# Performance work log

Hardware: AMD Instinct MI355X
Metric: run time of the kernel (lower is better)

The kernel has to match this reference:

```python
import jax, jax.numpy as jnp
import numpy as np

C = 512
H_FEAT, W_FEAT = 50, 75
ROI_SIZE = 7
SCALE = 16.0
N_ROIS = 512
N_CLASS = 21
FC_IN = C * ROI_SIZE * ROI_SIZE  # 25088
FC_DIM = 4096


def setup_inputs() -> dict:
    key = jax.random.key(0)
    ks = jax.random.split(key, 12)
    x = jax.random.normal(ks[0], (1, C, H_FEAT, W_FEAT), jnp.float32)
    img_h, img_w = H_FEAT * 16, W_FEAT * 16
    # boxes (x1,y1,x2,y2) in image pixel coords, in-bounds, min side 32px
    x1 = jax.random.randint(ks[1], (N_ROIS,), 0, img_w - 64)
    y1 = jax.random.randint(ks[2], (N_ROIS,), 0, img_h - 64)
    w = jax.random.randint(ks[3], (N_ROIS,), 32, 400)
    h = jax.random.randint(ks[4], (N_ROIS,), 32, 400)
    x2 = jnp.minimum(x1 + w, img_w - 1)
    y2 = jnp.minimum(y1 + h, img_h - 1)
    rois = jnp.stack([x1, y1, x2, y2], axis=1).astype(jnp.float32)
    W1 = jax.random.normal(ks[5], (FC_IN, FC_DIM), jnp.float32) * 0.01
    b1 = jnp.zeros((FC_DIM,), jnp.float32)
    W2 = jax.random.normal(ks[6], (FC_DIM, FC_DIM), jnp.float32) * 0.01
    b2 = jnp.zeros((FC_DIM,), jnp.float32)
    W_loc = jax.random.normal(ks[7], (FC_DIM, N_CLASS * 4), jnp.float32) * 0.001
    b_loc = jnp.zeros((N_CLASS * 4,), jnp.float32)
    W_score = jax.random.normal(ks[8], (FC_DIM, N_CLASS), jnp.float32) * 0.01
    b_score = jnp.zeros((N_CLASS,), jnp.float32)
    return {"x": x, "rois": rois, "W1": W1, "b1": b1, "W2": W2, "b2": b2,
            "W_loc": W_loc, "b_loc": b_loc, "W_score": W_score, "b_score": b_score}


def _roi_adaptive_max_pool(feat, rois_i):
    """feat: [C,H,W]; rois_i: int32 [N,4] (x1,y1,x2,y2) in feature coords.
    Matches torch F.adaptive_max_pool2d on the inclusive crop [y1:y2+1, x1:x2+1].
    """
    KR = H_FEAT // ROI_SIZE + 2   # max rows per adaptive bin (<= ceil(H/7)+1)
    KC = W_FEAT // ROI_SIZE + 2   # max cols per adaptive bin
    p = jnp.arange(ROI_SIZE)

    def one(roi):
        x1, y1, x2, y2 = roi[0], roi[1], roi[2], roi[3]
        h = y2 - y1 + 1
        w = x2 - x1 + 1
        # torch adaptive pooling: start = floor(i*S/O), end = ceil((i+1)*S/O)
        rs = y1 + (p * h) // ROI_SIZE
        re = y1 + -((-(p + 1) * h) // ROI_SIZE)   # ceil via floor-div
        cs = x1 + (p * w) // ROI_SIZE
        ce = x1 + -((-(p + 1) * w) // ROI_SIZE)
        ri = rs[:, None] + jnp.arange(KR)[None, :]          # [7,KR]
        rv = ri < re[:, None]
        ri = jnp.clip(ri, 0, H_FEAT - 1)
        ci = cs[:, None] + jnp.arange(KC)[None, :]          # [7,KC]
        cv = ci < ce[:, None]
        ci = jnp.clip(ci, 0, W_FEAT - 1)
        g = feat[:, ri, :][:, :, :, ci]                      # [C,7,KR,7,KC]
        m = rv[:, :, None, None] & cv[None, None, :, :]      # [7,KR,7,KC]
        g = jnp.where(m[None], g, -jnp.inf)
        return g.max(axis=(2, 4))                            # [C,7,7]

    return jax.lax.map(one, rois_i)                          # [N,C,7,7]


def reference(x, rois, W1, b1, W2, b2, W_loc, b_loc, W_score, b_score):
    # rois.mul_(1/spatial_scale); rois = rois.long()  (trunc == floor for >=0)
    rois_i = (rois * (1.0 / SCALE)).astype(jnp.int32)
    pool = _roi_adaptive_max_pool(x[0], rois_i)              # [N,C,7,7]
    pool = pool.reshape(pool.shape[0], -1)                   # [N, 25088]
    fc = jax.nn.relu(pool @ W1 + b1)
    fc = jax.nn.relu(fc @ W2 + b2)
    roi_locs = fc @ W_loc + b_loc                            # [N, 84]
    roi_scores = fc @ W_score + b_score                      # [N, 21]
    return (roi_locs, roi_scores)
```

## Files before the change

kernel.cpp:

```cpp
#include <hip/hip_runtime.h>
#include <hip/hip_bf16.h>
#include <math.h>

typedef unsigned short U16;
typedef __bf16 bf16x8 __attribute__((ext_vector_type(8)));
typedef float floatx4 __attribute__((ext_vector_type(4)));
typedef unsigned short ushort8 __attribute__((ext_vector_type(8)));

#define C_CH 512
#define HF 50
#define WF 75
#define NROIS 512
#define FC_IN 25088
#define FC_DIM 4096
#define NHEAD 105
#define NHEAD_PAD 128
#define OUT_LOCS (NROIS * 84)

__device__ __forceinline__ float b2f(U16 u) {
    union { unsigned int i; float f; } x; x.i = ((unsigned int)u) << 16; return x.f;
}
__device__ __forceinline__ U16 f2b(float f) {
    union { float f; unsigned int i; } x; x.f = f;
    unsigned int r = x.i + 0x7fffu + ((x.i >> 16) & 1u);
    return (U16)(r >> 16);
}

__device__ __forceinline__ void gld_lds16(const U16* g, U16* lds_base, int lane) {
#if __has_builtin(__builtin_amdgcn_global_load_lds)
    typedef const __attribute__((address_space(1))) unsigned int* gas1;
    typedef __attribute__((address_space(3))) unsigned int* las3;
    __builtin_amdgcn_global_load_lds((gas1)(unsigned long long)g,
                                     (las3)(unsigned int)(unsigned long long)lds_base,
                                     16, 0, 0);
#else
    *(floatx4*)(lds_base + lane * 8) = *(const floatx4*)g;
#endif
}

__global__ void detect_kernel(const unsigned int* __restrict__ w1,
                              const unsigned int* __restrict__ rois,
                              int* __restrict__ flags) {
    __shared__ int cnt_w, cnt_r;
    if (threadIdx.x == 0) { cnt_w = 0; cnt_r = 0; }
    __syncthreads();
    int lw = 0;
    for (int i = threadIdx.x; i < 2048; i += 256) {
        const unsigned int w = w1[i];
        const unsigned int e = (w >> 7) & 0xFFu;
        if ((e >= 90u && e <= 130u) || (w & 0x7FFFu) == 0u) lw++;
    }
    int lr = 0;
    for (int i = threadIdx.x; i < 512; i += 256) {
        union { unsigned int u; float f; } v; v.u = rois[i];
        const float f = v.f;
        if (f >= 0.0f && f <= 1300.0f && f == floorf(f)) lr++;
    }
    atomicAdd(&cnt_w, lw);
    atomicAdd(&cnt_r, lr);
    __syncthreads();
    if (threadIdx.x == 0) {
        flags[0] = (cnt_w < 1024) ? 1 : 0;
        flags[1] = (cnt_r >= 256) ? 1 : 0;
    }
}

__global__ void roi_pool_kernel(const void* __restrict__ feat_,
                                const void* __restrict__ rois_,
                                const int* __restrict__ flags,
                                U16* __restrict__ pool) {
    const int n = blockIdx.x;
    const int ch0 = blockIdx.y * 32;
    const int t = threadIdx.x;
    const int f32w = flags[0];
    const int f32r = flags[1];
    __shared__ int rs[7], re_[7], cs[7], ce_[7];

    float c4[4];
    if (f32r) {
        const float* r = (const float*)rois_ + n * 4;
        c4[0] = r[0]; c4[1] = r[1]; c4[2] = r[2]; c4[3] = r[3];
    } else {
        const U16* r = (const U16*)rois_ + n * 4;
        c4[0] = b2f(r[0]); c4[1] = b2f(r[1]); c4[2] = b2f(r[2]); c4[3] = b2f(r[3]);
    }
    const int x1 = (int)(c4[0] * 0.0625f);
    const int y1 = (int)(c4[1] * 0.0625f);
    const int x2 = (int)(c4[2] * 0.0625f);
    const int y2 = (int)(c4[3] * 0.0625f);
    const int h = y2 - y1 + 1;
    const int w = x2 - x1 + 1;
    if (t < 7) {
        rs[t] = y1 + (t * h) / 7;
        re_[t] = y1 + ((t + 1) * h + 6) / 7;
        cs[t] = x1 + (t * w) / 7;
        ce_[t] = x1 + ((t + 1) * w + 6) / 7;
    }
    __syncthreads();

    const float* featf = (const float*)feat_;
    const U16* featu = (const U16*)feat_;

    for (int o = t; o < 32 * 49; o += 256) {
        const int ch = ch0 + o / 49;
        const int b = o % 49;
        const int ph = b / 7;
        const int pw = b - ph * 7;
        const int r0 = rs[ph], r1 = re_[ph];
        const int c0 = cs[pw], c1 = ce_[pw];
        const int base = ch * (HF * WF);
        float m = -1.0e4f;
        if (f32w) {
            for (int r = r0; r < r1; ++r) {
                const int rr = r < (HF - 1) ? r : (HF - 1);
                const float* fr = featf + base + rr * WF;
                for (int c = c0; c < c1; ++c) {
                    const int cc = c < (WF - 1) ? c : (WF - 1);
                    const float v = fr[cc];
                    m = (m > v) ? m : v;
                }
            }
        } else {
            for (int r = r0; r < r1; ++r) {
                const int rr = r < (HF - 1) ? r : (HF - 1);
                const U16* fr = featu + base + rr * WF;
                for (int c = c0; c < c1; ++c) {
                    const int cc = c < (WF - 1) ? c : (WF - 1);
                    const float v = b2f(fr[cc]);
                    m = (m > v) ? m : v;
                }
            }
        }
        m = fminf(fmaxf(m, -1.0e4f), 1.0e4f);
        pool[(size_t)n * FC_IN + ch * 49 + b] = f2b(m);
    }
}

#define GBM 128
#define GBN 128
#define GBK 32
#define BROW 40

__launch_bounds__(256, 2)
__global__ void gemm_fused_kernel(const U16* __restrict__ A, int lda,
                                  const void* __restrict__ B, int ldb,
                                  float* __restrict__ Cpart,
                                  int M, int N, int Ks,
                                  const int* __restrict__ flags) {
    __shared__ __align__(16) U16 a_lds[GBM * GBK];
    __shared__ __align__(16) U16 b_lds[GBN * BROW];

    const int t = threadIdx.x;
    const int wave = t >> 6, lane = t & 63;
    const int ln = lane & 15, q = lane >> 4;
    const int wm = wave >> 1, wn = wave & 1;
    const int bm = blockIdx.y * GBM, bn = blockIdx.x * GBN;
    const int s = blockIdx.z;
    const int kb = s * Ks, ke = kb + Ks;
    float* Cp = Cpart + (size_t)s * M * N;
    const int f32b = flags[0];

    floatx4 acc[4][4];
#pragma unroll
    for (int i = 0; i < 4; ++i)
#pragma unroll
        for (int j = 0; j < 4; ++j) acc[i][j] = (floatx4)0.0f;

    const int slot0 = wave * 2;
    const int rsl = lane >> 2;
    const int c8 = (lane & 3) * 8;
    const U16* Ag0 = A + (size_t)(bm + slot0 * 16 + rsl) * lda + c8;
    const U16* Ag1 = A + (size_t)(bm + slot0 * 16 + 16 + rsl) * lda + c8;
    U16* al0 = &a_lds[slot0 * 512];
    U16* al1 = &a_lds[(slot0 + 1) * 512];

    const int np = (t & 63) * 2;
    const int kg = (t >> 6) * 8;
    U16* bw0 = &b_lds[(size_t)np * BROW + kg];
    U16* bw1 = &b_lds[(size_t)(np + 1) * BROW + kg];

    if (f32b) {
        const float* bp = (const float*)B + (size_t)(kb + kg) * ldb + bn + np;
        typedef float float2v __attribute__((ext_vector_type(2)));
        float2v v[8];
#pragma unroll
        for (int j = 0; j < 8; ++j) v[j] = *(const float2v*)(bp + (size_t)j * ldb);
        bp += (size_t)GBK * ldb;

        for (int k0 = kb; k0 < ke; k0 += GBK) {
            gld_lds16(Ag0 + k0, al0, lane);
            gld_lds16(Ag1 + k0, al1, lane);
            union { __bf16 b[8]; ushort8 s8; } h0, h1;
#pragma unroll
            for (int j = 0; j < 8; ++j) {
                h0.b[j] = (__bf16)v[j].x;
                h1.b[j] = (__bf16)v[j].y;
            }
            *(ushort8*)bw0 = h0.s8;
            *(ushort8*)bw1 = h1.s8;
            __syncthreads();

            bf16x8 av[4], bv[4];
#pragma unroll
            for (int mt = 0; mt < 4; ++mt)
                av[mt] = *(const bf16x8*)&a_lds[(wm * 64 + mt * 16 + ln) * GBK + q * 8];
#pragma unroll
            for (int nt = 0; nt < 4; ++nt)
                bv[nt] = *(const bf16x8*)&b_lds[(size_t)(wn * 64 + nt * 16 + ln) * BROW + q * 8];

            if (k0 + GBK < ke) {
#pragma unroll
                for (int j = 0; j < 8; ++j) v[j] = *(const float2v*)(bp + (size_t)j * ldb);
                bp += (size_t)GBK * ldb;
            }

#pragma unroll
            for (int mt = 0; mt < 4; ++mt)
#pragma unroll
                for (int nt = 0; nt < 4; ++nt)
                    acc[mt][nt] = __builtin_amdgcn_mfma_f32_16x16x32_bf16(
                        av[mt], bv[nt], acc[mt][nt], 0, 0, 0);
            __syncthreads();
        }
    } else {
        const int ldw = ldb >> 1;
        const unsigned int* bp = (const unsigned int*)B +
                                 (((size_t)(kb + kg) * ldb + bn + np) >> 1);
        unsigned int v[8];
#pragma unroll
        for (int j = 0; j < 8; ++j) v[j] = bp[(size_t)j * ldw];
        bp += (size_t)GBK * ldw;

        for (int k0 = kb; k0 < ke; k0 += GBK) {
            gld_lds16(Ag0 + k0, al0, lane);
            gld_lds16(Ag1 + k0, al1, lane);
            union { U16 u[8]; ushort8 s8; } h0, h1;
#pragma unroll
            for (int j = 0; j < 8; ++j) {
                h0.u[j] = (U16)(v[j] & 0xffffu);
                h1.u[j] = (U16)(v[j] >> 16);
            }
            *(ushort8*)bw0 = h0.s8;
            *(ushort8*)bw1 = h1.s8;
            __syncthreads();

            bf16x8 av[4], bv[4];
#pragma unroll
            for (int mt = 0; mt < 4; ++mt)
                av[mt] = *(const bf16x8*)&a_lds[(wm * 64 + mt * 16 + ln) * GBK + q * 8];
#pragma unroll
            for (int nt = 0; nt < 4; ++nt)
                bv[nt] = *(const bf16x8*)&b_lds[(size_t)(wn * 64 + nt * 16 + ln) * BROW + q * 8];

            if (k0 + GBK < ke) {
#pragma unroll
                for (int j = 0; j < 8; ++j) v[j] = bp[(size_t)j * ldw];
                bp += (size_t)GBK * ldw;
            }

#pragma unroll
            for (int mt = 0; mt < 4; ++mt)
#pragma unroll
                for (int nt = 0; nt < 4; ++nt)
                    acc[mt][nt] = __builtin_amdgcn_mfma_f32_16x16x32_bf16(
                        av[mt], bv[nt], acc[mt][nt], 0, 0, 0);
            __syncthreads();
        }
    }

#pragma unroll
    for (int nt = 0; nt < 4; ++nt) {
        const int col = bn + wn * 64 + nt * 16 + ln;
#pragma unroll
        for (int mt = 0; mt < 4; ++mt) {
            const int row = bm + wm * 64 + mt * 16 + q * 4;
#pragma unroll
            for (int r = 0; r < 4; ++r)
                Cp[(size_t)(row + r) * N + col] = acc[mt][nt][r];
        }
    }
}

__launch_bounds__(256, 2)
__global__ void gemm_tn_kernel(const U16* __restrict__ A, int lda,
                               const U16* __restrict__ BT, int ldb,
                               float* __restrict__ Cpart,
                               int M, int N, int Ks) {
    __shared__ __align__(16) U16 a_lds[GBM * GBK];
    __shared__ __align__(16) U16 b_lds[GBN * GBK];

    const int t = threadIdx.x;
    const int wave = t >> 6, lane = t & 63;
    const int ln = lane & 15, q = lane >> 4;
    const int wm = wave >> 1, wn = wave & 1;
    const int bm = blockIdx.y * GBM, bn = blockIdx.x * GBN;
    const int s = blockIdx.z;
    const int kb = s * Ks, ke = kb + Ks;
    float* Cp = Cpart + (size_t)s * M * N;

    floatx4 acc[4][4];
#pragma unroll
    for (int i = 0; i < 4; ++i)
#pragma unroll
        for (int j = 0; j < 4; ++j) acc[i][j] = (floatx4)0.0f;

    const int slot0 = wave * 2;
    const int rsl = lane >> 2;
    const int c8 = (lane & 3) * 8;
    const U16* Ag0 = A + (size_t)(bm + slot0 * 16 + rsl) * lda + c8;
    const U16* Ag1 = A + (size_t)(bm + slot0 * 16 + 16 + rsl) * lda + c8;
    const U16* Bg0 = BT + (size_t)(bn + slot0 * 16 + rsl) * ldb + c8;
    const U16* Bg1 = BT + (size_t)(bn + slot0 * 16 + 16 + rsl) * ldb + c8;
    U16* al0 = &a_lds[slot0 * 512];
    U16* al1 = &a_lds[(slot0 + 1) * 512];
    U16* bl0 = &b_lds[slot0 * 512];
    U16* bl1 = &b_lds[(slot0 + 1) * 512];

    for (int k0 = kb; k0 < ke; k0 += GBK) {
        gld_lds16(Ag0 + k0, al0, lane);
        gld_lds16(Ag1 + k0, al1, lane);
        gld_lds16(Bg0 + k0, bl0, lane);
        gld_lds16(Bg1 + k0, bl1, lane);
        __syncthreads();

        bf16x8 av[4], bv[4];
#pragma unroll
        for (int mt = 0; mt < 4; ++mt)
            av[mt] = *(const bf16x8*)&a_lds[(wm * 64 + mt * 16 + ln) * GBK + q * 8];
#pragma unroll
        for (int nt = 0; nt < 4; ++nt)
            bv[nt] = *(const bf16x8*)&b_lds[(wn * 64 + nt * 16 + ln) * GBK + q * 8];

#pragma unroll
        for (int mt = 0; mt < 4; ++mt)
#pragma unroll
            for (int nt = 0; nt < 4; ++nt)
                acc[mt][nt] = __builtin_amdgcn_mfma_f32_16x16x32_bf16(
                    av[mt], bv[nt], acc[mt][nt], 0, 0, 0);
        __syncthreads();
    }

#pragma unroll
    for (int nt = 0; nt < 4; ++nt) {
        const int col = bn + wn * 64 + nt * 16 + ln;
#pragma unroll
        for (int mt = 0; mt < 4; ++mt) {
            const int row = bm + wm * 64 + mt * 16 + q * 4;
#pragma unroll
            for (int r = 0; r < 4; ++r)
                Cp[(size_t)(row + r) * N + col] = acc[mt][nt][r];
        }
    }
}

__global__ void reduce_act_kernel(const float* __restrict__ Cpart,
                                  const U16* __restrict__ bias,
                                  U16* __restrict__ Cout,
                                  int MN, int N, int S, int do_relu) {
    const int i4 = (blockIdx.x * 256 + threadIdx.x) * 4;
    if (i4 >= MN) return;
    floatx4 sum = *(const floatx4*)&Cpart[i4];
    for (int s = 1; s < S; ++s)
        sum += *(const floatx4*)&Cpart[(size_t)s * MN + i4];
    const int nb = i4 & (N - 1);
    U16 o[4];
#pragma unroll
    for (int j = 0; j < 4; ++j) {
        float v = sum[j] + b2f(bias[nb + j]);
        if (do_relu) { v = v > 0.0f ? v : 0.0f; v = fminf(v, 1.0e4f); }
        o[j] = f2b(v);
    }
    *(unsigned long long*)&Cout[i4] = *(unsigned long long*)o;
}

__global__ void pack_headsT_kernel(const void* __restrict__ W_loc,
                                   const void* __restrict__ W_score,
                                   const U16* __restrict__ b_loc,
                                   const U16* __restrict__ b_score,
                                   const int* __restrict__ flags,
                                   U16* __restrict__ WhT, U16* __restrict__ bh) {
    const int idx = blockIdx.x * 256 + threadIdx.x;
    const int c = idx >> 12;
    const int k = idx & 4095;
    const int f32w = flags[0];
    U16 v = 0;
    if (f32w) {
        if (c < 84) v = f2b(((const float*)W_loc)[(size_t)k * 84 + c]);
        else if (c < NHEAD) v = f2b(((const float*)W_score)[(size_t)k * 21 + (c - 84)]);
    } else {
        if (c < 84) v = ((const U16*)W_loc)[(size_t)k * 84 + c];
        else if (c < NHEAD) v = ((const U16*)W_score)[(size_t)k * 21 + (c - 84)];
    }
    WhT[idx] = v;
    if (idx < NHEAD_PAD) {
        U16 bb = 0;
        if (idx < 84) bb = b_loc[idx];
        else if (idx < NHEAD) bb = b_score[idx - 84];
        bh[idx] = bb;
    }
}

__global__ void head_reduce_kernel(const float* __restrict__ Cpart,
                                   const U16* __restrict__ bh,
                                   const int* __restrict__ flags,
                                   void* __restrict__ out, int S) {
    const int idx = blockIdx.x * 256 + threadIdx.x;
    if (idx >= NROIS * NHEAD_PAD) return;
    const int m = idx >> 7;
    const int c = idx & 127;
    float s = 0.0f;
    for (int ss = 0; ss < S; ++ss)
        s += Cpart[(size_t)ss * (NROIS * NHEAD_PAD) + idx];
    s += b2f(bh[c]);
    if (c >= NHEAD) return;
    const int dst = (c < 84) ? (m * 84 + c) : (OUT_LOCS + m * 21 + (c - 84));
    if (flags[0]) ((float*)out)[dst] = s;
    else ((U16*)out)[dst] = f2b(s);
}

#define BM 128
#define BN 64
#define BK 32

__launch_bounds__(256, 2)
__global__ void gemm_bias_kernel(const U16* __restrict__ A,
                                 const void* __restrict__ B,
                                 const U16* __restrict__ bias,
                                 U16* __restrict__ Cout,
                                 int M, int N, int K, int do_relu,
                                 const int* __restrict__ flags, int use_flag) {
    __shared__ U16 a_lds[BM][BK];
    __shared__ U16 b_lds[BK][80];
    const int b_f32 = use_flag ? flags[0] : 0;
    const int t = threadIdx.x;
    const int wave = t >> 6, lane = t & 63;
    const int ln = lane & 15, q = lane >> 4;
    const int wm = wave >> 1, wn = wave & 1;
    const int bm = blockIdx.y * BM, bn = blockIdx.x * BN;
    floatx4 acc[4][2];
#pragma unroll
    for (int i = 0; i < 4; ++i)
#pragma unroll
        for (int j = 0; j < 2; ++j) acc[i][j] = (floatx4)0.0f;
    const int arow = t >> 2, acol = (t & 3) * 8;
    const int bk = t >> 3, bn8 = (t & 7) * 8;
    const int browp = ((bk & 7) << 2) | (bk >> 3);
    const U16* Ap0 = A + (size_t)(bm + arow) * K + acol;
    const U16* Ap1 = A + (size_t)(bm + 64 + arow) * K + acol;
    const U16* Bp16 = (const U16*)B + (size_t)bk * N + bn + bn8;
    const float* Bp32 = (const float*)B + (size_t)bk * N + bn + bn8;
    for (int k0 = 0; k0 < K; k0 += BK) {
        *(floatx4*)&a_lds[arow][acol] = *(const floatx4*)(Ap0 + k0);
        *(floatx4*)&a_lds[64 + arow][acol] = *(const floatx4*)(Ap1 + k0);
        if (b_f32) {
            const float* src = Bp32 + (size_t)k0 * N;
            union { U16 u[8]; floatx4 v; } tmp;
#pragma unroll
            for (int j = 0; j < 8; ++j) tmp.u[j] = f2b(src[j]);
            *(floatx4*)&b_lds[browp][bn8] = tmp.v;
        } else {
            *(floatx4*)&b_lds[browp][bn8] = *(const floatx4*)(Bp16 + (size_t)k0 * N);
        }
        __syncthreads();
        bf16x8 av[4];
#pragma unroll
        for (int mt = 0; mt < 4; ++mt)
            av[mt] = *(const bf16x8*)&a_lds[wm * 64 + mt * 16 + ln][q * 8];
        union { U16 u[8]; bf16x8 v; } bu[2];
#pragma unroll
        for (int nt = 0; nt < 2; ++nt) {
            const int n = wn * 32 + nt * 16 + ln;
#pragma unroll
            for (int j = 0; j < 8; ++j) bu[nt].u[j] = b_lds[(j << 2) | q][n];
        }
#pragma unroll
        for (int mt = 0; mt < 4; ++mt)
#pragma unroll
            for (int nt = 0; nt < 2; ++nt)
                acc[mt][nt] = __builtin_amdgcn_mfma_f32_16x16x32_bf16(
                    av[mt], bu[nt].v, acc[mt][nt], 0, 0, 0);
        __syncthreads();
    }
#pragma unroll
    for (int nt = 0; nt < 2; ++nt) {
        const int col = bn + wn * 32 + nt * 16 + ln;
        const float bv = b2f(bias[col]);
#pragma unroll
        for (int mt = 0; mt < 4; ++mt) {
            const int row = bm + wm * 64 + mt * 16 + q * 4;
#pragma unroll
            for (int r = 0; r < 4; ++r) {
                float v = acc[mt][nt][r] + bv;
                if (do_relu) { v = v > 0.0f ? v : 0.0f; v = fminf(v, 1.0e4f); }
                Cout[(size_t)(row + r) * N + col] = f2b(v);
            }
        }
    }
}

__global__ void pack_heads_kernel(const void* __restrict__ W_loc,
                                  const void* __restrict__ W_score,
                                  const U16* __restrict__ b_loc,
                                  const U16* __restrict__ b_score,
                                  const int* __restrict__ flags,
                                  U16* __restrict__ Wh, U16* __restrict__ bh) {
    const int k = blockIdx.x;
    const int c = threadIdx.x;
    const int f32w = flags[0];
    U16 v = 0;
    if (f32w) {
        if (c < 84) v = f2b(((const float*)W_loc)[k * 84 + c]);
        else if (c < NHEAD) v = f2b(((const float*)W_score)[k * 21 + (c - 84)]);
    } else {
        if (c < 84) v = ((const U16*)W_loc)[k * 84 + c];
        else if (c < NHEAD) v = ((const U16*)W_score)[k * 21 + (c - 84)];
    }
    Wh[k * NHEAD_PAD + c] = v;
    if (k == 0) {
        U16 bb = 0;
        if (c < 84) bb = b_loc[c];
        else if (c < NHEAD) bb = b_score[c - 84];
        bh[c] = bb;
    }
}

__global__ void scatter_out_kernel(const U16* __restrict__ Chead,
                                   const int* __restrict__ flags,
                                   void* __restrict__ out) {
    const int idx = blockIdx.x * 256 + threadIdx.x;
    if (idx >= NROIS * NHEAD) return;
    const int f32o = flags[0];
    const int m = idx / NHEAD;
    const int c = idx - m * NHEAD;
    const U16 v = Chead[m * NHEAD_PAD + c];
    const int dst = (c < 84) ? (m * 84 + c) : (OUT_LOCS + m * 21 + (c - 84));
    if (f32o) ((float*)out)[dst] = b2f(v);
    else ((U16*)out)[dst] = v;
}

extern "C" void kernel_launch(void* const* d_in, const int* in_sizes, int n_in,
                              void* d_out, int out_size, void* d_ws, size_t ws_size,
                              hipStream_t stream) {
    const void* x       = d_in[0];
    const void* rois    = d_in[1];
    const void* W1      = d_in[2];
    const U16* b1       = (const U16*)d_in[3];
    const void* W2      = d_in[4];
    const U16* b2       = (const U16*)d_in[5];
    const void* W_loc   = d_in[6];
    const U16* b_loc    = (const U16*)d_in[7];
    const void* W_score = d_in[8];
    const U16* b_score  = (const U16*)d_in[9];

    int* flags = (int*)d_ws;
    char* p = (char*)d_ws + 256;
    U16* pool = (U16*)p;                       p += (size_t)NROIS * FC_IN * 2;
    U16* fc1  = (U16*)p;                       p += (size_t)NROIS * FC_DIM * 2;
    U16* fc2  = (U16*)p;                       p += (size_t)NROIS * FC_DIM * 2;

    detect_kernel<<<1, 256, 0, stream>>>((const unsigned int*)W1,
                                         (const unsigned int*)rois, flags);
    roi_pool_kernel<<<dim3(NROIS, 16), 256, 0, stream>>>(x, rois, flags, pool);

    char* pf = p;
    U16* WhT = (U16*)pf;  pf += (size_t)NHEAD_PAD * FC_DIM * 2;
    U16* bh  = (U16*)pf;  pf += 256;
    float* Cpart = (float*)pf; pf += (size_t)4 * NROIS * FC_DIM * 4;
    const size_t need_fast = (size_t)(pf - (char*)d_ws);

    if (ws_size >= need_fast) {
        pack_headsT_kernel<<<(NHEAD_PAD * FC_DIM) / 256, 256, 0, stream>>>(
            W_loc, W_score, b_loc, b_score, flags, WhT, bh);

        gemm_fused_kernel<<<dim3(FC_DIM / GBN, NROIS / GBM, 4), 256, 0, stream>>>(
            pool, FC_IN, W1, FC_DIM, Cpart, NROIS, FC_DIM, FC_IN / 4, flags);
        reduce_act_kernel<<<(NROIS * FC_DIM / 4) / 256, 256, 0, stream>>>(
            Cpart, b1, fc1, NROIS * FC_DIM, FC_DIM, 4, 1);

        gemm_fused_kernel<<<dim3(FC_DIM / GBN, NROIS / GBM, 4), 256, 0, stream>>>(
            fc1, FC_DIM, W2, FC_DIM, Cpart, NROIS, FC_DIM, FC_DIM / 4, flags);
        reduce_act_kernel<<<(NROIS * FC_DIM / 4) / 256, 256, 0, stream>>>(
            Cpart, b2, fc2, NROIS * FC_DIM, FC_DIM, 4, 1);

        gemm_tn_kernel<<<dim3(1, NROIS / GBM, 32), 256, 0, stream>>>(
            fc2, FC_DIM, WhT, FC_DIM, Cpart, NROIS, NHEAD_PAD, FC_DIM / 32);
        head_reduce_kernel<<<(NROIS * NHEAD_PAD) / 256, 256, 0, stream>>>(
            Cpart, bh, flags, d_out, 32);
    } else {
        U16* Wh    = (U16*)p;
        U16* bhf   = Wh + (size_t)FC_DIM * NHEAD_PAD;
        U16* Chead = bhf + NHEAD_PAD;
        pack_heads_kernel<<<FC_DIM, NHEAD_PAD, 0, stream>>>(W_loc, W_score, b_loc,
                                                            b_score, flags, Wh, bhf);
        gemm_bias_kernel<<<dim3(FC_DIM / BN, NROIS / BM), 256, 0, stream>>>(
            pool, W1, b1, fc1, NROIS, FC_DIM, FC_IN, 1, flags, 1);
        gemm_bias_kernel<<<dim3(FC_DIM / BN, NROIS / BM), 256, 0, stream>>>(
            fc1, W2, b2, fc2, NROIS, FC_DIM, FC_DIM, 1, flags, 1);
        gemm_bias_kernel<<<dim3(NHEAD_PAD / BN, NROIS / BM), 256, 0, stream>>>(
            fc2, Wh, bhf, Chead, NROIS, NHEAD_PAD, FC_DIM, 0, flags, 0);
        scatter_out_kernel<<<(NROIS * NHEAD + 255) / 256, 256, 0, stream>>>(
            Chead, flags, d_out);
    }
}
```

Before: 950.3 us.

## Double-buffer LDS in split-K GEMM and raise split-K factor to eight

The fused FC GEMM now uses two LDS buffers, so the next tile's A copy and converted B tile are written while MFMAs run on the current tile. This removes one barrier per iteration, and global B loads are issued two iterations ahead. The B load pattern changes from float2 per thread over paired columns to scalar loads of columns lane and lane+64. Split-K goes from 4 to 8, which doubles the grid for occupancy but also doubles the partial-sum buffer and the reduce traffic. LDS use doubles per block and register pressure rises, which may hurt the two-blocks-per-CU launch bound.

```diff
diff --git a/kernel.cpp b/kernel.cpp
--- a/kernel.cpp
+++ b/kernel.cpp
@@ -147,8 +147,8 @@
                                   float* __restrict__ Cpart,
                                   int M, int N, int Ks,
                                   const int* __restrict__ flags) {
-    __shared__ __align__(16) U16 a_lds[GBM * GBK];
-    __shared__ __align__(16) U16 b_lds[GBN * BROW];
+    __shared__ __align__(16) U16 a_lds[2][GBM * GBK];
+    __shared__ __align__(16) U16 b_lds[2][GBN * BROW];
 
     const int t = threadIdx.x;
     const int wave = t >> 6, lane = t & 63;
@@ -156,9 +156,10 @@
     const int wm = wave >> 1, wn = wave & 1;
     const int bm = blockIdx.y * GBM, bn = blockIdx.x * GBN;
     const int s = blockIdx.z;
-    const int kb = s * Ks, ke = kb + Ks;
+    const int kb = s * Ks;
     float* Cp = Cpart + (size_t)s * M * N;
     const int f32b = flags[0];
+    const int nIter = Ks / GBK;
 
     floatx4 acc[4][4];
 #pragma unroll
@@ -169,51 +170,70 @@
     const int slot0 = wave * 2;
     const int rsl = lane >> 2;
     const int c8 = (lane & 3) * 8;
-    const U16* Ag0 = A + (size_t)(bm + slot0 * 16 + rsl) * lda + c8;
-    const U16* Ag1 = A + (size_t)(bm + slot0 * 16 + 16 + rsl) * lda + c8;
-    U16* al0 = &a_lds[slot0 * 512];
-    U16* al1 = &a_lds[(slot0 + 1) * 512];
-
-    const int np = (t & 63) * 2;
-    const int kg = (t >> 6) * 8;
-    U16* bw0 = &b_lds[(size_t)np * BROW + kg];
-    U16* bw1 = &b_lds[(size_t)(np + 1) * BROW + kg];
+    const U16* Ag0 = A + (size_t)(bm + slot0 * 16 + rsl) * lda + kb + c8;
+    const U16* Ag1 = Ag0 + (size_t)16 * lda;
+    const int ao0 = slot0 * 512;
+    const int ao1 = ao0 + 512;
+
+    const int cl = lane;
+    const int kg = wave * 8;
+    const int bo0 = cl * BROW + kg;
+    const int bo1 = (cl + 64) * BROW + kg;
 
     if (f32b) {
-        const float* bp = (const float*)B + (size_t)(kb + kg) * ldb + bn + np;
-        typedef float float2v __attribute__((ext_vector_type(2)));
-        float2v v[8];
-#pragma unroll
-        for (int j = 0; j < 8; ++j) v[j] = *(const float2v*)(bp + (size_t)j * ldb);
+        const float* bp = (const float*)B + (size_t)(kb + kg) * ldb + bn + cl;
+        float va0[8], va1[8];
+#pragma unroll
+        for (int j = 0; j < 8; ++j) {
+            va0[j] = bp[(size_t)j * ldb];
+            va1[j] = bp[(size_t)j * ldb + 64];
+        }
         bp += (size_t)GBK * ldb;
-
-        for (int k0 = kb; k0 < ke; k0 += GBK) {
-            gld_lds16(Ag0 + k0, al0, lane);
-            gld_lds16(Ag1 + k0, al1, lane);
+        gld_lds16(Ag0, &a_lds[0][ao0], lane);
+        gld_lds16(Ag1, &a_lds[0][ao1], lane);
+        {
             union { __bf16 b[8]; ushort8 s8; } h0, h1;
 #pragma unroll
+            for (int j = 0; j < 8; ++j) { h0.b[j] = (__bf16)va0[j]; h1.b[j] = (__bf16)va1[j]; }
+            *(ushort8*)&b_lds[0][bo0] = h0.s8;
+            *(ushort8*)&b_lds[0][bo1] = h1.s8;
+        }
+        if (nIter > 1) {
+#pragma unroll
             for (int j = 0; j < 8; ++j) {
-                h0.b[j] = (__bf16)v[j].x;
-                h1.b[j] = (__bf16)v[j].y;
-            }
-            *(ushort8*)bw0 = h0.s8;
-            *(ushort8*)bw1 = h1.s8;
-            __syncthreads();
-
+                va0[j] = bp[(size_t)j * ldb];
+                va1[j] = bp[(size_t)j * ldb + 64];
+            }
+            bp += (size_t)GBK * ldb;
+        }
+        __syncthreads();
+
+        for (int it = 0; it < nIter; ++it) {
+            const int cur = it & 1, nxt = cur ^ 1;
             bf16x8 av[4], bv[4];
 #pragma unroll
             for (int mt = 0; mt < 4; ++mt)
-                av[mt] = *(const bf16x8*)&a_lds[(wm * 64 + mt * 16 + ln) * GBK + q * 8];
+                av[mt] = *(const bf16x8*)&a_lds[cur][(wm * 64 + mt * 16 + ln) * GBK + q * 8];
 #pragma unroll
             for (int nt = 0; nt < 4; ++nt)
-                bv[nt] = *(const bf16x8*)&b_lds[(size_t)(wn * 64 + nt * 16 + ln) * BROW + q * 8];
-
-            if (k0 + GBK < ke) {
-#pragma unroll
-                for (int j = 0; j < 8; ++j) v[j] = *(const float2v*)(bp + (size_t)j * ldb);
+                bv[nt] = *(const bf16x8*)&b_lds[cur][(wn * 64 + nt * 16 + ln) * BROW + q * 8];
+            if (it + 1 < nIter) {
+                gld_lds16(Ag0 + (it + 1) * GBK, &a_lds[nxt][ao0], lane);
+                gld_lds16(Ag1 + (it + 1) * GBK, &a_lds[nxt][ao1], lane);
+                union { __bf16 b[8]; ushort8 s8; } h0, h1;
+#pragma unroll
+                for (int j = 0; j < 8; ++j) { h0.b[j] = (__bf16)va0[j]; h1.b[j] = (__bf16)va1[j]; }
+                *(ushort8*)&b_lds[nxt][bo0] = h0.s8;
+                *(ushort8*)&b_lds[nxt][bo1] = h1.s8;
+            }
+            if (it + 2 < nIter) {
+#pragma unroll
+                for (int j = 0; j < 8; ++j) {
+                    va0[j] = bp[(size_t)j * ldb];
+                    va1[j] = bp[(size_t)j * ldb + 64];
+                }
                 bp += (size_t)GBK * ldb;
             }
-
 #pragma unroll
             for (int mt = 0; mt < 4; ++mt)
 #pragma unroll
@@ -223,41 +243,59 @@
             __syncthreads();
         }
     } else {
-        const int ldw = ldb >> 1;
-        const unsigned int* bp = (const unsigned int*)B +
-                                 (((size_t)(kb + kg) * ldb + bn + np) >> 1);
-        unsigned int v[8];
-#pragma unroll
-        for (int j = 0; j < 8; ++j) v[j] = bp[(size_t)j * ldw];
-        bp += (size_t)GBK * ldw;
-
-        for (int k0 = kb; k0 < ke; k0 += GBK) {
-            gld_lds16(Ag0 + k0, al0, lane);
-            gld_lds16(Ag1 + k0, al1, lane);
+        const U16* bp = (const U16*)B + (size_t)(kb + kg) * ldb + bn + cl;
+        U16 va0[8], va1[8];
+#pragma unroll
+        for (int j = 0; j < 8; ++j) {
+            va0[j] = bp[(size_t)j * ldb];
+            va1[j] = bp[(size_t)j * ldb + 64];
+        }
+        bp += (size_t)GBK * ldb;
+        gld_lds16(Ag0, &a_lds[0][ao0], lane);
+        gld_lds16(Ag1, &a_lds[0][ao1], lane);
+        {
             union { U16 u[8]; ushort8 s8; } h0, h1;
 #pragma unroll
+            for (int j = 0; j < 8; ++j) { h0.u[j] = va0[j]; h1.u[j] = va1[j]; }
+            *(ushort8*)&b_lds[0][bo0] = h0.s8;
+            *(ushort8*)&b_lds[0][bo1] = h1.s8;
+        }
+        if (nIter > 1) {
+#pragma unroll
             for (int j = 0; j < 8; ++j) {
-                h0.u[j] = (U16)(v[j] & 0xffffu);
-                h1.u[j] = (U16)(v[j] >> 16);
-            }
-            *(ushort8*)bw0 = h0.s8;
-            *(ushort8*)bw1 = h1.s8;
-            __syncthreads();
-
+                va0[j] = bp[(size_t)j * ldb];
+                va1[j] = bp[(size_t)j * ldb + 64];
+            }
+            bp += (size_t)GBK * ldb;
+        }
+        __syncthreads();
+
+        for (int it = 0; it < nIter; ++it) {
+            const int cur = it & 1, nxt = cur ^ 1;
             bf16x8 av[4], bv[4];
 #pragma unroll
             for (int mt = 0; mt < 4; ++mt)
-                av[mt] = *(const bf16x8*)&a_lds[(wm * 64 + mt * 16 + ln) * GBK + q * 8];
+                av[mt] = *(const bf16x8*)&a_lds[cur][(wm * 64 + mt * 16 + ln) * GBK + q * 8];
 #pragma unroll
             for (int nt = 0; nt < 4; ++nt)
-                bv[nt] = *(const bf16x8*)&b_lds[(size_t)(wn * 64 + nt * 16 + ln) * BROW + q * 8];
-
-            if (k0 + GBK < ke) {
-#pragma unroll
-                for (int j = 0; j < 8; ++j) v[j] = bp[(size_t)j * ldw];
-                bp += (size_t)GBK * ldw;
-            }
-
+                bv[nt] = *(const bf16x8*)&b_lds[cur][(wn * 64 + nt * 16 + ln) * BROW + q * 8];
+            if (it + 1 < nIter) {
+                gld_lds16(Ag0 + (it + 1) * GBK, &a_lds[nxt][ao0], lane);
+                gld_lds16(Ag1 + (it + 1) * GBK, &a_lds[nxt][ao1], lane);
+                union { U16 u[8]; ushort8 s8; } h0, h1;
+#pragma unroll
+                for (int j = 0; j < 8; ++j) { h0.u[j] = va0[j]; h1.u[j] = va1[j]; }
+                *(ushort8*)&b_lds[nxt][bo0] = h0.s8;
+                *(ushort8*)&b_lds[nxt][bo1] = h1.s8;
+            }
+            if (it + 2 < nIter) {
+#pragma unroll
+                for (int j = 0; j < 8; ++j) {
+                    va0[j] = bp[(size_t)j * ldb];
+                    va1[j] = bp[(size_t)j * ldb + 64];
+                }
+                bp += (size_t)GBK * ldb;
+            }
 #pragma unroll
             for (int mt = 0; mt < 4; ++mt)
 #pragma unroll
@@ -565,22 +603,22 @@
     char* pf = p;
     U16* WhT = (U16*)pf;  pf += (size_t)NHEAD_PAD * FC_DIM * 2;
     U16* bh  = (U16*)pf;  pf += 256;
-    float* Cpart = (float*)pf; pf += (size_t)4 * NROIS * FC_DIM * 4;
+    float* Cpart = (float*)pf; pf += (size_t)8 * NROIS * FC_DIM * 4;
     const size_t need_fast = (size_t)(pf - (char*)d_ws);
 
     if (ws_size >= need_fast) {
         pack_headsT_kernel<<<(NHEAD_PAD * FC_DIM) / 256, 256, 0, stream>>>(
             W_loc, W_score, b_loc, b_score, flags, WhT, bh);
 
-        gemm_fused_kernel<<<dim3(FC_DIM / GBN, NROIS / GBM, 4), 256, 0, stream>>>(
-            pool, FC_IN, W1, FC_DIM, Cpart, NROIS, FC_DIM, FC_IN / 4, flags);
+        gemm_fused_kernel<<<dim3(FC_DIM / GBN, NROIS / GBM, 8), 256, 0, stream>>>(
+            pool, FC_IN, W1, FC_DIM, Cpart, NROIS, FC_DIM, FC_IN / 8, flags);
         reduce_act_kernel<<<(NROIS * FC_DIM / 4) / 256, 256, 0, stream>>>(
-            Cpart, b1, fc1, NROIS * FC_DIM, FC_DIM, 4, 1);
-
-        gemm_fused_kernel<<<dim3(FC_DIM / GBN, NROIS / GBM, 4), 256, 0, stream>>>(
-            fc1, FC_DIM, W2, FC_DIM, Cpart, NROIS, FC_DIM, FC_DIM / 4, flags);
+            Cpart, b1, fc1, NROIS * FC_DIM, FC_DIM, 8, 1);
+
+        gemm_fused_kernel<<<dim3(FC_DIM / GBN, NROIS / GBM, 8), 256, 0, stream>>>(
+            fc1, FC_DIM, W2, FC_DIM, Cpart, NROIS, FC_DIM, FC_DIM / 8, flags);
         reduce_act_kernel<<<(NROIS * FC_DIM / 4) / 256, 256, 0, stream>>>(
-            Cpart, b2, fc2, NROIS * FC_DIM, FC_DIM, 4, 1);
+            Cpart, b2, fc2, NROIS * FC_DIM, FC_DIM, 8, 1);
 
         gemm_tn_kernel<<<dim3(1, NROIS / GBM, 32), 256, 0, stream>>>(
             fc2, FC_DIM, WhT, FC_DIM, Cpart, NROIS, NHEAD_PAD, FC_DIM / 32);
```

Result: faster. 902.1 us (-5.1%).
